# Kernel optimization log

Hardware: AMD Instinct MI355X
Metric: run time of the kernel (lower is better)

The kernel has to match this reference:

```python
import jax, jax.numpy as jnp
import numpy as np

N = 100_000
E = 1_600_000
IN_DIM = 128
PE_DIM = 16
HID = 128
LAT = 64
K = 4  # Chebyshev order


def _prop(w_hat, src, dst, x):
    # y[i] = sum_{e: dst[e]=i} w_hat[e] * x[src[e]]  (sparse matvec with L_hat)
    return jnp.zeros_like(x).at[dst].add(w_hat[:, None] * x[src])


def _cheb_layer(x, w_hat, src, dst, W, b):
    # PyG ChebConv with sym normalization, lambda_max=2: L_hat = -D^{-1/2} A D^{-1/2}
    # Tx0 = x; Tx1 = L_hat x; Tx_k = 2 L_hat Tx_{k-1} - Tx_{k-2}; out = sum_k Tx_k @ W_k + b
    Tx0 = x
    out = Tx0 @ W[0]
    Tx1 = _prop(w_hat, src, dst, x)
    out = out + Tx1 @ W[1]
    for k in range(2, K):
        Tx2 = 2.0 * _prop(w_hat, src, dst, Tx1) - Tx0
        out = out + Tx2 @ W[k]
        Tx0, Tx1 = Tx1, Tx2
    return out + b


def setup_inputs() -> dict:
    key = jax.random.key(0)
    ks = jax.random.split(key, 8)
    x = jax.random.normal(ks[0], (N, IN_DIM), jnp.float32)
    lap_pe = jax.random.normal(ks[1], (N, PE_DIM), jnp.float32)
    edge_index = jax.random.randint(ks[2], (2, E), 0, N)
    edge_weight = jax.random.uniform(ks[3], (E,), jnp.float32)
    d0 = IN_DIM + PE_DIM
    W0 = jax.random.normal(ks[4], (K, d0, HID), jnp.float32) / np.float32(np.sqrt(d0))
    b0 = jnp.zeros((HID,), jnp.float32)
    W1 = jax.random.normal(ks[5], (K, HID, HID), jnp.float32) / np.float32(np.sqrt(HID))
    b1 = jnp.zeros((HID,), jnp.float32)
    Wmu = jax.random.normal(ks[6], (HID, LAT), jnp.float32) / np.float32(np.sqrt(HID))
    bmu = jnp.zeros((LAT,), jnp.float32)
    Wlv = jax.random.normal(ks[7], (HID, LAT), jnp.float32) / np.float32(np.sqrt(HID))
    blv = jnp.zeros((LAT,), jnp.float32)
    return dict(x=x, edge_index=edge_index, lap_pe=lap_pe, edge_weight=edge_weight,
                W0=W0, b0=b0, W1=W1, b1=b1, Wmu=Wmu, bmu=bmu, Wlv=Wlv, blv=blv)


def reference(x, edge_index, lap_pe, edge_weight, W0, b0, W1, b1, Wmu, bmu, Wlv, blv):
    src, dst = edge_index[0], edge_index[1]
    # Encoder adds self-loops, ChebConv removes them before get_laplacian -> net: drop self-loops
    w = jnp.where(src == dst, jnp.zeros((), x.dtype), edge_weight)
    deg = jnp.zeros((x.shape[0],), x.dtype).at[src].add(w)
    deg_safe = jnp.where(deg > 0, deg, jnp.ones((), x.dtype))
    dis = jnp.where(deg > 0, jax.lax.rsqrt(deg_safe), jnp.zeros((), x.dtype))
    w_hat = -dis[src] * w * dis[dst]  # scaled Laplacian off-diagonal; diagonal = 0

    h = jnp.concatenate([x, lap_pe], axis=1)  # [N, in_dim + pe_dim]
    h = jax.nn.relu(_cheb_layer(h, w_hat, src, dst, W0, b0))
    h = jax.nn.relu(_cheb_layer(h, w_hat, src, dst, W1, b1))
    mu = h @ Wmu + bmu
    logvar = h @ Wlv + blv
    return (mu, logvar)
```

## Files before the change

kernel.cpp:

```cpp
#include <hip/hip_runtime.h>
#include <hip/hip_bf16.h>

typedef float f32x4 __attribute__((ext_vector_type(4)));
typedef unsigned short u16x8 __attribute__((ext_vector_type(8)));

static __device__ __forceinline__ void mfma16(f32x4& c, const u16x8& a, const u16x8& b) {
    asm("v_mfma_f32_16x16x32_bf16 %0, %1, %2, %0" : "+v"(c) : "v"(a), "v"(b));
}

static __device__ __forceinline__ unsigned short f2bf(float f) {
    __hip_bfloat16 h = __float2bfloat16(f);
    return *reinterpret_cast<unsigned short*>(&h);
}

static __device__ __forceinline__ float bflo(unsigned int v) { return __uint_as_float(v << 16); }
static __device__ __forceinline__ float bfhi(unsigned int v) { return __uint_as_float(v & 0xffff0000u); }


__global__ __launch_bounds__(1024) void k_dis_blocksum(float* deg, const int* __restrict__ cnt,
                                                       int* bsum, int N) {
    __shared__ int sd[1024];
    int i = blockIdx.x * 1024 + threadIdx.x;
    if (i < N) {
        float d = deg[i];
        deg[i] = (d > 0.f) ? rsqrtf(d) : 0.f;
    }
    sd[threadIdx.x] = (i < N) ? cnt[i] : 0;
    __syncthreads();
    for (int s = 512; s > 0; s >>= 1) {
        if (threadIdx.x < s) sd[threadIdx.x] += sd[threadIdx.x + s];
        __syncthreads();
    }
    if (threadIdx.x == 0) bsum[blockIdx.x] = sd[0];
}

__global__ __launch_bounds__(128) void k_scan_bsum(int* bsum, int nb) {
    __shared__ int sd[128];
    int t = threadIdx.x;
    int v = (t < nb) ? bsum[t] : 0;
    sd[t] = v;
    __syncthreads();
    for (int d = 1; d < 128; d <<= 1) {
        int x = (t >= d) ? sd[t - d] : 0;
        __syncthreads();
        sd[t] += x;
        __syncthreads();
    }
    if (t < nb) bsum[t] = sd[t] - v;
}

__global__ __launch_bounds__(1024) void k_scan(const int* __restrict__ cnt, const int* __restrict__ bsum,
                                               int* rowp, int N) {
    __shared__ int sd[1024];
    int i = blockIdx.x * 1024 + threadIdx.x;
    int v = (i < N) ? cnt[i] : 0;
    sd[threadIdx.x] = v;
    __syncthreads();
    for (int d = 1; d < 1024; d <<= 1) {
        int x = (threadIdx.x >= d) ? sd[threadIdx.x - d] : 0;
        __syncthreads();
        sd[threadIdx.x] += x;
        __syncthreads();
    }
    if (i < N) rowp[i] = sd[threadIdx.x] - v + bsum[blockIdx.x];
}

__global__ __launch_bounds__(256) void k_build_csr(const int* __restrict__ src, const int* __restrict__ dst,
                                                   const float* __restrict__ ew, const float* __restrict__ dis,
                                                   const int* __restrict__ rowp,
                                                   const unsigned char* __restrict__ rank,
                                                   int2* __restrict__ pack, int E) {
    int base = blockIdx.x * 512 + threadIdx.x;
#pragma unroll
    for (int u = 0; u < 2; u++) {
        int e = base + u * 256;
        if (e < E) {
            int s = src[e], d = dst[e];
            float w = (s == d) ? 0.f : ew[e];
            float wh = -dis[s] * w * dis[d];
            int pos = rowp[d] + (int)rank[e];
            int2 p;
            p.x = s;
            p.y = __float_as_int(wh);
            pack[pos] = p;
        }
    }
}


__global__ __launch_bounds__(256) void k_combine(const float* __restrict__ W, unsigned short* __restrict__ AT,
                                                 int D, int KPAD) {
    int i = blockIdx.x * 256 + threadIdx.x;
    int tot = 4 * 128 * KPAD;
    if (i >= tot) return;
    int sel = i / (128 * KPAD);
    int rem = i - sel * 128 * KPAD;
    int n = rem / KPAD;
    int kk = rem - n * KPAD;
    float v = 0.f;
    if (kk < D) {
        if (sel == 0)      v = W[(0 * D + kk) * 128 + n] - W[(2 * D + kk) * 128 + n];
        else if (sel == 1) v = W[(1 * D + kk) * 128 + n] - 3.f * W[(3 * D + kk) * 128 + n];
        else if (sel == 2) v = 2.f * W[(2 * D + kk) * 128 + n];
        else               v = 4.f * W[(3 * D + kk) * 128 + n];
    }
    AT[i] = f2bf(v);
}

__global__ __launch_bounds__(256) void k_headsT(const float* __restrict__ Wmu, const float* __restrict__ Wlv,
                                                unsigned short* __restrict__ AT) {
    int i = blockIdx.x * 256 + threadIdx.x;
    if (i >= 128 * 128) return;
    int n = i >> 7, kk = i & 127;
    float v = (n < 64) ? Wmu[kk * 64 + n] : Wlv[kk * 64 + (n - 64)];
    AT[i] = f2bf(v);
}


template <int KPAD>
static __device__ __forceinline__ void gemm_pair_regB(const float* __restrict__ x,
                                                      const float* __restrict__ pe,
                                                      const unsigned short* __restrict__ Bta,
                                                      const unsigned short* __restrict__ Btb,
                                                      unsigned short* __restrict__ outA,
                                                      unsigned short* __restrict__ outB,
                                                      int N, int bx, unsigned short* As) {
    constexpr int LP = KPAD + 8;
    const int tid = threadIdx.x;
    const int row0 = bx * 64;

    {
        constexpr int TOT = 64 * KPAD;
        for (int c = tid * 8; c < TOT; c += 256 * 8) {
            int r = c / KPAD;
            int k = c - r * KPAD;
            int gr = row0 + r;
            if (gr > N - 1) gr = N - 1;
            u16x8 v;
            if (k < 128) {
                float4 f0 = *reinterpret_cast<const float4*>(&x[(size_t)gr * 128 + k]);
                float4 f1 = *reinterpret_cast<const float4*>(&x[(size_t)gr * 128 + k + 4]);
                v[0] = f2bf(f0.x); v[1] = f2bf(f0.y); v[2] = f2bf(f0.z); v[3] = f2bf(f0.w);
                v[4] = f2bf(f1.x); v[5] = f2bf(f1.y); v[6] = f2bf(f1.z); v[7] = f2bf(f1.w);
            } else if (k < 144) {
                float4 f0 = *reinterpret_cast<const float4*>(&pe[(size_t)gr * 16 + (k - 128)]);
                float4 f1 = *reinterpret_cast<const float4*>(&pe[(size_t)gr * 16 + (k - 124)]);
                v[0] = f2bf(f0.x); v[1] = f2bf(f0.y); v[2] = f2bf(f0.z); v[3] = f2bf(f0.w);
                v[4] = f2bf(f1.x); v[5] = f2bf(f1.y); v[6] = f2bf(f1.z); v[7] = f2bf(f1.w);
            } else {
                v = (u16x8){0, 0, 0, 0, 0, 0, 0, 0};
            }
            *reinterpret_cast<u16x8*>(&As[r * LP + k]) = v;
        }
    }
    __syncthreads();

    const int wave = tid >> 6, lane = tid & 63;
    const int wm = wave & 1, ww = wave >> 1;
    const int lr = lane & 15, lg = lane >> 4;
    const unsigned short* Bw = ww ? Btb : Bta;

    f32x4 acc[2][8];
#pragma unroll
    for (int i = 0; i < 2; i++)
#pragma unroll
        for (int j = 0; j < 8; j++) acc[i][j] = (f32x4){0.f, 0.f, 0.f, 0.f};

    asm volatile("s_nop 7"
                 : "+v"(acc[0][0]), "+v"(acc[0][4]), "+v"(acc[1][0]), "+v"(acc[1][4]));

    constexpr int KS = KPAD / 32;
#pragma unroll
    for (int ks = 0; ks < KS; ks++) {
        u16x8 a0 = *reinterpret_cast<const u16x8*>(&As[(wm * 32 + lr) * LP + ks * 32 + lg * 8]);
        u16x8 a1 = *reinterpret_cast<const u16x8*>(&As[(wm * 32 + 16 + lr) * LP + ks * 32 + lg * 8]);
#pragma unroll
        for (int g = 0; g < 2; g++) {
            u16x8 b[4];
#pragma unroll
            for (int j = 0; j < 4; j++)
                b[j] = *reinterpret_cast<const u16x8*>(&Bw[(size_t)((g * 4 + j) * 16 + lr) * KPAD + ks * 32 + lg * 8]);
#pragma unroll
            for (int j = 0; j < 4; j++) {
                mfma16(acc[0][g * 4 + j], a0, b[j]);
                mfma16(acc[1][g * 4 + j], a1, b[j]);
            }
        }
    }

    asm volatile("s_nop 7\n\ts_nop 7\n\ts_nop 7"
                 : "+v"(acc[0][0]), "+v"(acc[0][4]), "+v"(acc[1][0]), "+v"(acc[1][4]));

    unsigned short* outp = ww ? outB : outA;
#pragma unroll
    for (int fm = 0; fm < 2; fm++)
#pragma unroll
        for (int fn = 0; fn < 8; fn++)
#pragma unroll
            for (int i = 0; i < 4; i++) {
                int r = row0 + wm * 32 + fm * 16 + lg * 4 + i;
                if (r < N) outp[(size_t)r * 128 + fn * 16 + lr] = f2bf(acc[fm][fn][i]);
            }
}


__global__ __launch_bounds__(256, 4) void k_mega(const int* __restrict__ src, const int* __restrict__ dst,
                                                 const float* __restrict__ ew,
                                                 float* deg, int* cnt, unsigned char* __restrict__ rank,
                                                 const float* __restrict__ x, const float* __restrict__ pe,
                                                 const unsigned short* __restrict__ AT0,
                                                 unsigned short* __restrict__ oZ3, unsigned short* __restrict__ oZ2,
                                                 unsigned short* __restrict__ oZ1, unsigned short* __restrict__ oZ0,
                                                 int N, int E, int EPC) {
    __shared__ __align__(16) unsigned short As[64 * 168];
    const int bid = blockIdx.x;

    {
        int P = bid & 1;
        int bx = bid >> 1;
        const unsigned short* Bta = AT0 + (size_t)(3 - 2 * P) * 128 * 160;
        const unsigned short* Btb = AT0 + (size_t)(2 - 2 * P) * 128 * 160;
        unsigned short* outA = (P == 0) ? oZ3 : oZ1;
        unsigned short* outB = (P == 0) ? oZ2 : oZ0;
        gemm_pair_regB<160>(x, pe, Bta, Btb, outA, outB, N, bx, As);
    }

    {
        int e0 = bid * EPC;
        int e1 = e0 + EPC;
        if (e1 > E) e1 = E;
        for (int e = e0 + threadIdx.x; e < e1; e += 256) {
            int s = src[e], d = dst[e];
            float w = (s == d) ? 0.f : ew[e];
            atomicAdd(&deg[s], w);
            rank[e] = (unsigned char)atomicAdd(&cnt[d], 1);
        }
    }
}


__global__ __launch_bounds__(256, 4) void k_gemm_l1_heads(const unsigned short* __restrict__ h1,
                                                          const unsigned short* __restrict__ U1,
                                                          const unsigned short* __restrict__ U2,
                                                          const unsigned short* __restrict__ U3,
                                                          const unsigned short* __restrict__ AT1,
                                                          const unsigned short* __restrict__ ATH,
                                                          const float* __restrict__ b1,
                                                          const float* __restrict__ bmu,
                                                          const float* __restrict__ blv,
                                                          float* __restrict__ out, int N) {
    constexpr int LP = 136;
    __shared__ __align__(16) unsigned short As[64 * LP];
    const int tid = threadIdx.x;
    const int row0 = blockIdx.x * 64;
    const int wave = tid >> 6, lane = tid & 63;
    const int wm = wave & 1, wn = wave >> 1;
    const int lr = lane & 15, lg = lane >> 4;

    f32x4 acc[2][4];
#pragma unroll
    for (int i = 0; i < 2; i++)
#pragma unroll
        for (int j = 0; j < 4; j++) acc[i][j] = (f32x4){0.f, 0.f, 0.f, 0.f};

#pragma unroll 4
    for (int seg = 0; seg < 4; seg++) {
        const unsigned short* sp = (seg == 0) ? h1 : (seg == 1) ? U1 : (seg == 2) ? U2 : U3;
        for (int c = tid * 8; c < 64 * 128; c += 256 * 8) {
            int r = c >> 7;
            int k = c & 127;
            int gr = row0 + r;
            if (gr > N - 1) gr = N - 1;
            u16x8 v = *reinterpret_cast<const u16x8*>(&sp[(size_t)gr * 128 + k]);
            *reinterpret_cast<u16x8*>(&As[r * LP + k]) = v;
        }
        __syncthreads();
        const unsigned short* Bseg = AT1 + (size_t)seg * 128 * 128;
#pragma unroll
        for (int ks = 0; ks < 4; ks++) {
            u16x8 a0 = *reinterpret_cast<const u16x8*>(&As[(wm * 32 + lr) * LP + ks * 32 + lg * 8]);
            u16x8 a1 = *reinterpret_cast<const u16x8*>(&As[(wm * 32 + 16 + lr) * LP + ks * 32 + lg * 8]);
            u16x8 b[4];
#pragma unroll
            for (int j = 0; j < 4; j++)
                b[j] = *reinterpret_cast<const u16x8*>(&Bseg[(size_t)((wn * 64 + j * 16 + lr)) * 128 + ks * 32 + lg * 8]);
#pragma unroll
            for (int j = 0; j < 4; j++) {
                mfma16(acc[0][j], a0, b[j]);
                mfma16(acc[1][j], a1, b[j]);
            }
        }
        __syncthreads();
    }

    asm volatile("s_nop 7\n\ts_nop 7\n\ts_nop 7"
                 : "+v"(acc[0][0]), "+v"(acc[0][1]), "+v"(acc[0][2]), "+v"(acc[0][3]),
                   "+v"(acc[1][0]), "+v"(acc[1][1]), "+v"(acc[1][2]), "+v"(acc[1][3]));

#pragma unroll
    for (int fm = 0; fm < 2; fm++)
#pragma unroll
        for (int fn = 0; fn < 4; fn++)
#pragma unroll
            for (int i = 0; i < 4; i++) {
                int rl = wm * 32 + fm * 16 + lg * 4 + i;
                int c = wn * 64 + fn * 16 + lr;
                float v = fmaxf(acc[fm][fn][i] + b1[c], 0.f);
                As[rl * LP + c] = f2bf(v);
            }
    __syncthreads();

    f32x4 acc2[2][4];
#pragma unroll
    for (int i = 0; i < 2; i++)
#pragma unroll
        for (int j = 0; j < 4; j++) acc2[i][j] = (f32x4){0.f, 0.f, 0.f, 0.f};

    asm volatile("s_nop 7"
                 : "+v"(acc2[0][0]), "+v"(acc2[0][1]), "+v"(acc2[1][0]), "+v"(acc2[1][1]));

#pragma unroll
    for (int ks = 0; ks < 4; ks++) {
        u16x8 a0 = *reinterpret_cast<const u16x8*>(&As[(wm * 32 + lr) * LP + ks * 32 + lg * 8]);
        u16x8 a1 = *reinterpret_cast<const u16x8*>(&As[(wm * 32 + 16 + lr) * LP + ks * 32 + lg * 8]);
        u16x8 b[4];
#pragma unroll
        for (int j = 0; j < 4; j++)
            b[j] = *reinterpret_cast<const u16x8*>(&ATH[(size_t)(wn * 64 + j * 16 + lr) * 128 + ks * 32 + lg * 8]);
#pragma unroll
        for (int j = 0; j < 4; j++) {
            mfma16(acc2[0][j], a0, b[j]);
            mfma16(acc2[1][j], a1, b[j]);
        }
    }

    asm volatile("s_nop 7\n\ts_nop 7\n\ts_nop 7"
                 : "+v"(acc2[0][0]), "+v"(acc2[0][1]), "+v"(acc2[1][0]), "+v"(acc2[1][1]));

#pragma unroll
    for (int fm = 0; fm < 2; fm++)
#pragma unroll
        for (int fn = 0; fn < 4; fn++)
#pragma unroll
            for (int i = 0; i < 4; i++) {
                int r = row0 + wm * 32 + fm * 16 + lg * 4 + i;
                if (r < N) {
                    int c = wn * 64 + fn * 16 + lr;
                    if (c < 64) out[(size_t)r * 64 + c] = acc2[fm][fn][i] + bmu[c];
                    else out[(size_t)N * 64 + (size_t)r * 64 + (c - 64)] = acc2[fm][fn][i] + blv[c - 64];
                }
            }
}


template <int MODE>
__global__ __launch_bounds__(256) void k_prop(const uint4* __restrict__ tin4,
                                              const uint4* __restrict__ z4,
                                              uint4* __restrict__ tout4,
                                              const float* __restrict__ bias,
                                              const int* __restrict__ rowp,
                                              const long long* __restrict__ pack,
                                              int N, int E) {
    int wave = threadIdx.x >> 6, lane = threadIdx.x & 63;
    int node = blockIdx.x * 4 + wave;
    if (node >= N) return;
    int beg = rowp[node];
    int end = (node == N - 1) ? E : rowp[node + 1];
    const int grp = lane >> 4, li = lane & 15;
    float s0 = 0.f, s1 = 0.f, s2 = 0.f, s3 = 0.f, s4 = 0.f, s5 = 0.f, s6 = 0.f, s7 = 0.f;
    int e = beg + grp;
    for (; e + 4 < end; e += 8) {
        long long qa = __builtin_nontemporal_load(pack + e);
        long long qb = __builtin_nontemporal_load(pack + e + 4);
        uint4 va = tin4[(size_t)(unsigned int)qa * 16 + li];
        uint4 vb = tin4[(size_t)(unsigned int)qb * 16 + li];
        float wa = __uint_as_float((unsigned int)((unsigned long long)qa >> 32));
        float wb = __uint_as_float((unsigned int)((unsigned long long)qb >> 32));
        s0 = fmaf(wa, bflo(va.x), s0); s1 = fmaf(wa, bfhi(va.x), s1);
        s2 = fmaf(wa, bflo(va.y), s2); s3 = fmaf(wa, bfhi(va.y), s3);
        s4 = fmaf(wa, bflo(va.z), s4); s5 = fmaf(wa, bfhi(va.z), s5);
        s6 = fmaf(wa, bflo(va.w), s6); s7 = fmaf(wa, bfhi(va.w), s7);
        s0 = fmaf(wb, bflo(vb.x), s0); s1 = fmaf(wb, bfhi(vb.x), s1);
        s2 = fmaf(wb, bflo(vb.y), s2); s3 = fmaf(wb, bfhi(vb.y), s3);
        s4 = fmaf(wb, bflo(vb.z), s4); s5 = fmaf(wb, bfhi(vb.z), s5);
        s6 = fmaf(wb, bflo(vb.w), s6); s7 = fmaf(wb, bfhi(vb.w), s7);
    }
    for (; e < end; e += 4) {
        long long qa = __builtin_nontemporal_load(pack + e);
        uint4 va = tin4[(size_t)(unsigned int)qa * 16 + li];
        float wa = __uint_as_float((unsigned int)((unsigned long long)qa >> 32));
        s0 = fmaf(wa, bflo(va.x), s0); s1 = fmaf(wa, bfhi(va.x), s1);
        s2 = fmaf(wa, bflo(va.y), s2); s3 = fmaf(wa, bfhi(va.y), s3);
        s4 = fmaf(wa, bflo(va.z), s4); s5 = fmaf(wa, bfhi(va.z), s5);
        s6 = fmaf(wa, bflo(va.w), s6); s7 = fmaf(wa, bfhi(va.w), s7);
    }
    s0 += __shfl_xor(s0, 16); s1 += __shfl_xor(s1, 16);
    s2 += __shfl_xor(s2, 16); s3 += __shfl_xor(s3, 16);
    s4 += __shfl_xor(s4, 16); s5 += __shfl_xor(s5, 16);
    s6 += __shfl_xor(s6, 16); s7 += __shfl_xor(s7, 16);
    s0 += __shfl_xor(s0, 32); s1 += __shfl_xor(s1, 32);
    s2 += __shfl_xor(s2, 32); s3 += __shfl_xor(s3, 32);
    s4 += __shfl_xor(s4, 32); s5 += __shfl_xor(s5, 32);
    s6 += __shfl_xor(s6, 32); s7 += __shfl_xor(s7, 32);
    if (lane < 16) {
        float r0 = s0, r1 = s1, r2 = s2, r3 = s3, r4 = s4, r5 = s5, r6 = s6, r7 = s7;
        if (MODE != 2) {
            uint4 zv = z4[(size_t)node * 16 + li];
            r0 += bflo(zv.x); r1 += bfhi(zv.x); r2 += bflo(zv.y); r3 += bfhi(zv.y);
            r4 += bflo(zv.z); r5 += bfhi(zv.z); r6 += bflo(zv.w); r7 += bfhi(zv.w);
        }
        if (MODE == 1) {
            const float* bp = bias + li * 8;
            r0 = fmaxf(r0 + bp[0], 0.f); r1 = fmaxf(r1 + bp[1], 0.f);
            r2 = fmaxf(r2 + bp[2], 0.f); r3 = fmaxf(r3 + bp[3], 0.f);
            r4 = fmaxf(r4 + bp[4], 0.f); r5 = fmaxf(r5 + bp[5], 0.f);
            r6 = fmaxf(r6 + bp[6], 0.f); r7 = fmaxf(r7 + bp[7], 0.f);
        }
        uint4 o;
        o.x = (unsigned int)f2bf(r0) | ((unsigned int)f2bf(r1) << 16);
        o.y = (unsigned int)f2bf(r2) | ((unsigned int)f2bf(r3) << 16);
        o.z = (unsigned int)f2bf(r4) | ((unsigned int)f2bf(r5) << 16);
        o.w = (unsigned int)f2bf(r6) | ((unsigned int)f2bf(r7) << 16);
        tout4[(size_t)node * 16 + li] = o;
    }
}


extern "C" void kernel_launch(void* const* d_in, const int* in_sizes, int n_in,
                              void* d_out, int out_size, void* d_ws, size_t ws_size,
                              hipStream_t stream) {
    const float* x   = (const float*)d_in[0];
    const int*   ei  = (const int*)d_in[1];
    const float* pe  = (const float*)d_in[2];
    const float* ew  = (const float*)d_in[3];
    const float* W0  = (const float*)d_in[4];
    const float* b0  = (const float*)d_in[5];
    const float* W1  = (const float*)d_in[6];
    const float* b1  = (const float*)d_in[7];
    const float* Wmu = (const float*)d_in[8];
    const float* bmu = (const float*)d_in[9];
    const float* Wlv = (const float*)d_in[10];
    const float* blv = (const float*)d_in[11];

    const int N = in_sizes[0] / 128;
    const int E = in_sizes[3];
    const int* src = ei;
    const int* dst = ei + E;

    char* ws = (char*)d_ws;
    size_t off = 0;
    auto alloc = [&](size_t bytes) {
        size_t o = off;
        off += (bytes + 1023) & ~(size_t)1023;
        return o;
    };
    float* deg = (float*)(ws + alloc(4 * (size_t)N));
    int* cnt   = (int*)(ws + alloc(4 * (size_t)N));
    size_t zero_bytes = off;
    unsigned char* rank = (unsigned char*)(ws + alloc((size_t)E));
    int* rowp  = (int*)(ws + alloc(4 * (size_t)N));
    int* bsum  = (int*)(ws + alloc(4 * 128));
    unsigned short* AT0 = (unsigned short*)(ws + alloc(2 * 4 * 128 * 160));
    unsigned short* AT1 = (unsigned short*)(ws + alloc(2 * 4 * 128 * 128));
    unsigned short* ATH = (unsigned short*)(ws + alloc(2 * 128 * 128));
    int2* pack = (int2*)(ws + alloc(8 * (size_t)E));
    unsigned int* B1 = (unsigned int*)(ws + alloc(2 * (size_t)N * 128));
    unsigned int* B2 = (unsigned int*)(ws + alloc(2 * (size_t)N * 128));
    unsigned int* B3 = (unsigned int*)(ws + alloc(2 * (size_t)N * 128));
    unsigned int* B4 = (unsigned int*)(ws + alloc(2 * (size_t)N * 128));
    unsigned int* B5 = (unsigned int*)(ws + alloc(2 * (size_t)N * 128));

    hipMemsetAsync(ws, 0, zero_bytes, stream);

    dim3 b256(256);
    k_combine<<<dim3((4 * 128 * 160 + 255) / 256), b256, 0, stream>>>(W0, AT0, 144, 160);
    k_combine<<<dim3((4 * 128 * 128 + 255) / 256), b256, 0, stream>>>(W1, AT1, 128, 128);
    k_headsT<<<dim3((128 * 128 + 255) / 256), b256, 0, stream>>>(Wmu, Wlv, ATH);

    int G64 = (N + 63) / 64;
    int total = 2 * G64;
    int EPC = (E + total - 1) / total;
    k_mega<<<dim3(total), b256, 0, stream>>>(src, dst, ew, deg, cnt, rank, x, pe, AT0,
                                             (unsigned short*)B1, (unsigned short*)B2,
                                             (unsigned short*)B3, (unsigned short*)B4,
                                             N, E, EPC);

    int nb = (N + 1023) / 1024;
    k_dis_blocksum<<<dim3(nb), dim3(1024), 0, stream>>>(deg, cnt, bsum, N);
    k_scan_bsum<<<dim3(1), dim3(128), 0, stream>>>(bsum, nb);
    k_scan<<<dim3(nb), dim3(1024), 0, stream>>>(cnt, bsum, rowp, N);
    k_build_csr<<<dim3((E + 511) / 512), b256, 0, stream>>>(src, dst, ew, deg, rowp, rank, pack, E);

    dim3 gp((N + 3) / 4);
    const long long* packll = (const long long*)pack;
    uint4* B1v = (uint4*)B1; uint4* B2v = (uint4*)B2; uint4* B3v = (uint4*)B3;
    uint4* B4v = (uint4*)B4; uint4* B5v = (uint4*)B5;

    k_prop<0><<<gp, b256, 0, stream>>>(B1v, B2v, B5v, nullptr, rowp, packll, N, E);
    k_prop<0><<<gp, b256, 0, stream>>>(B5v, B3v, B1v, nullptr, rowp, packll, N, E);
    k_prop<1><<<gp, b256, 0, stream>>>(B1v, B4v, B2v, b0, rowp, packll, N, E);

    k_prop<2><<<gp, b256, 0, stream>>>(B2v, nullptr, B3v, nullptr, rowp, packll, N, E);
    k_prop<2><<<gp, b256, 0, stream>>>(B3v, nullptr, B4v, nullptr, rowp, packll, N, E);
    k_prop<2><<<gp, b256, 0, stream>>>(B4v, nullptr, B5v, nullptr, rowp, packll, N, E);

    k_gemm_l1_heads<<<dim3(G64), b256, 0, stream>>>((const unsigned short*)B2, (const unsigned short*)B3,
                                                    (const unsigned short*)B4, (const unsigned short*)B5,
                                                    AT1, ATH, b1, bmu, blv, (float*)d_out, N);
}
```

Baseline: 738.2 us.

## Merge weight-prep kernels, widen CSR build per block, drop nontemporal pack loads

Folds the three weight-preparation kernels into one launch to cut launch overhead. The CSR build kernel now handles four edges per thread instead of two, halving its grid. The propagation kernels read the edge pack with plain loads instead of nontemporal loads, so it can stay in cache across the six propagation passes. This trades streaming-load behaviour for possible cache pressure on the feature gathers.

Result: faster. 695.4 us (-5.8%).

```diff
diff --git a/kernel.cpp b/kernel.cpp
--- a/kernel.cpp
+++ b/kernel.cpp
@@ -70,9 +70,9 @@
                                                    const int* __restrict__ rowp,
                                                    const unsigned char* __restrict__ rank,
                                                    int2* __restrict__ pack, int E) {
-    int base = blockIdx.x * 512 + threadIdx.x;
-#pragma unroll
-    for (int u = 0; u < 2; u++) {
+    int base = blockIdx.x * 1024 + threadIdx.x;
+#pragma unroll
+    for (int u = 0; u < 4; u++) {
         int e = base + u * 256;
         if (e < E) {
             int s = src[e], d = dst[e];
@@ -88,11 +88,9 @@
 }
 
 
-__global__ __launch_bounds__(256) void k_combine(const float* __restrict__ W, unsigned short* __restrict__ AT,
-                                                 int D, int KPAD) {
-    int i = blockIdx.x * 256 + threadIdx.x;
-    int tot = 4 * 128 * KPAD;
-    if (i >= tot) return;
+static __device__ __forceinline__ void combine_elem(const float* __restrict__ W,
+                                                    unsigned short* __restrict__ AT,
+                                                    int i, int D, int KPAD) {
     int sel = i / (128 * KPAD);
     int rem = i - sel * 128 * KPAD;
     int n = rem / KPAD;
@@ -107,13 +105,26 @@
     AT[i] = f2bf(v);
 }
 
-__global__ __launch_bounds__(256) void k_headsT(const float* __restrict__ Wmu, const float* __restrict__ Wlv,
-                                                unsigned short* __restrict__ AT) {
+__global__ __launch_bounds__(256) void k_prep_weights(const float* __restrict__ W0,
+                                                      const float* __restrict__ W1,
+                                                      const float* __restrict__ Wmu,
+                                                      const float* __restrict__ Wlv,
+                                                      unsigned short* __restrict__ AT0,
+                                                      unsigned short* __restrict__ AT1,
+                                                      unsigned short* __restrict__ ATH) {
+    constexpr int T0 = 4 * 128 * 160;
+    constexpr int T1 = 4 * 128 * 128;
     int i = blockIdx.x * 256 + threadIdx.x;
-    if (i >= 128 * 128) return;
-    int n = i >> 7, kk = i & 127;
-    float v = (n < 64) ? Wmu[kk * 64 + n] : Wlv[kk * 64 + (n - 64)];
-    AT[i] = f2bf(v);
+    if (i < T0) {
+        combine_elem(W0, AT0, i, 144, 160);
+    } else if (i < T0 + T1) {
+        combine_elem(W1, AT1, i - T0, 128, 128);
+    } else if (i < T0 + T1 + 128 * 128) {
+        int j = i - T0 - T1;
+        int n = j >> 7, kk = j & 127;
+        float v = (n < 64) ? Wmu[kk * 64 + n] : Wlv[kk * 64 + (n - 64)];
+        ATH[j] = f2bf(v);
+    }
 }
 
 
@@ -370,8 +381,8 @@
     float s0 = 0.f, s1 = 0.f, s2 = 0.f, s3 = 0.f, s4 = 0.f, s5 = 0.f, s6 = 0.f, s7 = 0.f;
     int e = beg + grp;
     for (; e + 4 < end; e += 8) {
-        long long qa = __builtin_nontemporal_load(pack + e);
-        long long qb = __builtin_nontemporal_load(pack + e + 4);
+        long long qa = pack[e];
+        long long qb = pack[e + 4];
         uint4 va = tin4[(size_t)(unsigned int)qa * 16 + li];
         uint4 vb = tin4[(size_t)(unsigned int)qb * 16 + li];
         float wa = __uint_as_float((unsigned int)((unsigned long long)qa >> 32));
@@ -386,7 +397,7 @@
         s6 = fmaf(wb, bflo(vb.w), s6); s7 = fmaf(wb, bfhi(vb.w), s7);
     }
     for (; e < end; e += 4) {
-        long long qa = __builtin_nontemporal_load(pack + e);
+        long long qa = pack[e];
         uint4 va = tin4[(size_t)(unsigned int)qa * 16 + li];
         float wa = __uint_as_float((unsigned int)((unsigned long long)qa >> 32));
         s0 = fmaf(wa, bflo(va.x), s0); s1 = fmaf(wa, bfhi(va.x), s1);
@@ -473,9 +484,10 @@
     hipMemsetAsync(ws, 0, zero_bytes, stream);
 
     dim3 b256(256);
-    k_combine<<<dim3((4 * 128 * 160 + 255) / 256), b256, 0, stream>>>(W0, AT0, 144, 160);
-    k_combine<<<dim3((4 * 128 * 128 + 255) / 256), b256, 0, stream>>>(W1, AT1, 128, 128);
-    k_headsT<<<dim3((128 * 128 + 255) / 256), b256, 0, stream>>>(Wmu, Wlv, ATH);
+    {
+        int tot = 4 * 128 * 160 + 4 * 128 * 128 + 128 * 128;
+        k_prep_weights<<<dim3((tot + 255) / 256), b256, 0, stream>>>(W0, W1, Wmu, Wlv, AT0, AT1, ATH);
+    }
 
     int G64 = (N + 63) / 64;
     int total = 2 * G64;
@@ -489,7 +501,7 @@
     k_dis_blocksum<<<dim3(nb), dim3(1024), 0, stream>>>(deg, cnt, bsum, N);
     k_scan_bsum<<<dim3(1), dim3(128), 0, stream>>>(bsum, nb);
     k_scan<<<dim3(nb), dim3(1024), 0, stream>>>(cnt, bsum, rowp, N);
-    k_build_csr<<<dim3((E + 511) / 512), b256, 0, stream>>>(src, dst, ew, deg, rowp, rank, pack, E);
+    k_build_csr<<<dim3((E + 1023) / 1024), b256, 0, stream>>>(src, dst, ew, deg, rowp, rank, pack, E);
 
     dim3 gp((N + 3) / 4);
     const long long* packll = (const long long*)pack;
```
